# Performance work log

Hardware: AMD Instinct MI355X
Metric: run time of the kernel (lower is better)

Reference implementation:

```python
import jax, jax.numpy as jnp
import numpy as np

STRIDE = (2, 2)
PADDING = (1, 1)
OUTPUT_PADDING = (0, 0)


def setup_inputs() -> dict:
    key = jax.random.key(0)
    k1, k2, k3 = jax.random.split(key, 3)
    B, Cin, H, W = 16, 32, 128, 128
    Cout, Kh, Kw = 32, 4, 4
    signal = jax.random.normal(k1, (B, Cin, H, W), dtype=jnp.float32)
    # conv_transpose weight layout: (Cin, Cout/groups, Kh, Kw)
    weight = jax.random.normal(k2, (Cin, Cout, Kh, Kw), dtype=jnp.float32) * 0.05
    bias = jax.random.normal(k3, (Cout,), dtype=jnp.float32)
    return {"signal": signal, "weight": weight, "bias": bias}


def reference(signal, weight, bias):
    """FFT-based 2D transposed convolution (stride 2, padding 1, groups=1, dilation=1).

    Matches torch.nn.functional.conv_transpose2d semantics:
      y[n] = sum_m x[m] * w[n - m*s], cropped by `padding` on each side.
    """
    sh, sw = STRIDE
    ph, pw = PADDING
    oph, opw = OUTPUT_PADDING
    B, Cin, H, W = signal.shape
    _, Cout, Kh, Kw = weight.shape

    # 1) zero-stuff the input by the stride (lhs dilation)
    Hu, Wu = (H - 1) * sh + 1, (W - 1) * sw + 1
    xu = jnp.zeros((B, Cin, Hu, Wu), dtype=signal.dtype)
    xu = xu.at[:, :, ::sh, ::sw].set(signal)

    # 2) full (true) convolution of upsampled signal with the weight via rFFT
    Nh, Nw = Hu + Kh - 1, Wu + Kw - 1  # full-conv output size == FFT size
    Xf = jnp.fft.rfft2(xu, s=(Nh, Nw))          # (B, Cin, Nh, Nw//2+1) complex64
    Wf = jnp.fft.rfft2(weight, s=(Nh, Nw))      # (Cin, Cout, Nh, Nw//2+1) complex64
    Yf = jnp.einsum('bihw,iohw->bohw', Xf, Wf)  # contract over input channels
    y = jnp.fft.irfft2(Yf, s=(Nh, Nw))          # (B, Cout, Nh, Nw) float32

    # 3) crop by padding; output_padding extends the end (zero here)
    out_h = (H - 1) * sh - 2 * ph + Kh + oph
    out_w = (W - 1) * sw - 2 * pw + Kw + opw
    y = y[:, :, ph:ph + out_h, pw:pw + out_w]

    # 4) bias
    return y + bias[None, :, None, None]
```

## Files before the change

### kernel.cpp

```cpp
#include <hip/hip_runtime.h>

#define B_    16
#define CIN   32
#define H_    128
#define W_    128
#define COUT  32
#define OH_   256
#define OW_   256

typedef __attribute__((ext_vector_type(8))) short bf8_t;
typedef __attribute__((ext_vector_type(4))) float f32x4;

__device__ inline unsigned int f2bf(float f) {
    unsigned int u = __float_as_uint(f);
    return (u + 0x7fffu + ((u >> 16) & 1u)) >> 16;
}

__global__ __launch_bounds__(256)
void prep_w(const float* __restrict__ wgt, unsigned short* __restrict__ wt) {
    int e = blockIdx.x * 256 + threadIdx.x;
    int khkw = e >> 10, co = (e >> 5) & 31, ci = e & 31;
    wt[e] = (unsigned short)f2bf(wgt[(ci * COUT + co) * 16 + khkw]);
}

__global__ __launch_bounds__(512)
void convt_fused(const float* __restrict__ x,
                 const unsigned short* __restrict__ wt,
                 const float* __restrict__ bias,
                 float* __restrict__ y) {
    __shared__ unsigned short xs[6 * 66 * 32];

    const int tid  = threadIdx.x;
    const int lane = tid & 63;
    const int wv   = tid >> 6;
    const int n    = blockIdx.z;
    const int t0   = blockIdx.y * 4;
    const int u0   = blockIdx.x * 64;

#pragma unroll
    for (int j = 0; j < 3; ++j) {
        const int c  = wv + j * 8;
        const int hr = c >> 2, gp = c & 3;
        const int ih = t0 - 1 + hr;
        const int iw = u0 - 1 + lane;
        const bool inb = ((unsigned)ih < H_) && ((unsigned)iw < W_);
        const float* xq = x + (((long)(n * CIN + gp * 8) * H_ + ih) * W_ + iw);
        float v[8];
#pragma unroll
        for (int k = 0; k < 8; ++k)
            v[k] = inb ? xq[(long)k * (H_ * W_)] : 0.0f;
        uint4 pk;
        pk.x = f2bf(v[0]) | (f2bf(v[1]) << 16);
        pk.y = f2bf(v[2]) | (f2bf(v[3]) << 16);
        pk.z = f2bf(v[4]) | (f2bf(v[5]) << 16);
        pk.w = f2bf(v[6]) | (f2bf(v[7]) << 16);
        const int slot = gp ^ ((iw >> 1) & 3);
        *(uint4*)(xs + (hr * 66 + lane) * 32 + slot * 8) = pk;
    }
    if (tid < 48) {
        const int c  = tid >> 1;
        const int hr = c >> 2, gp = c & 3;
        const int wc = 64 + (tid & 1);
        const int ih = t0 - 1 + hr;
        const int iw = u0 - 1 + wc;
        const bool inb = ((unsigned)ih < H_) && ((unsigned)iw < W_);
        const float* xq = x + (((long)(n * CIN + gp * 8) * H_ + ih) * W_ + iw);
        float v[8];
#pragma unroll
        for (int k = 0; k < 8; ++k)
            v[k] = inb ? xq[(long)k * (H_ * W_)] : 0.0f;
        uint4 pk;
        pk.x = f2bf(v[0]) | (f2bf(v[1]) << 16);
        pk.y = f2bf(v[2]) | (f2bf(v[3]) << 16);
        pk.z = f2bf(v[4]) | (f2bf(v[5]) << 16);
        pk.w = f2bf(v[6]) | (f2bf(v[7]) << 16);
        const int slot = gp ^ ((iw >> 1) & 3);
        *(uint4*)(xs + (hr * 66 + wc) * 32 + slot * 8) = pk;
    }

    const int ch   = wv & 1;
    const int trow = wv >> 1;
    const int g    = lane >> 4;
    const int li   = lane & 15;

    bf8_t wf[16];
    {
        const unsigned short* wp = wt + (ch * 16 + li) * 32 + g * 8;
#pragma unroll
        for (int kk = 0; kk < 16; ++kk)
            wf[kk] = *(const bf8_t*)(wp + kk * 1024);
    }
    float bias4[4];
#pragma unroll
    for (int r = 0; r < 4; ++r) bias4[r] = bias[ch * 16 + g * 4 + r];

    __syncthreads();

    const int t = t0 + trow;
#pragma unroll
    for (int st = 0; st < 4; ++st) {
        const int us = u0 + st * 16;

        bf8_t xf[3][3];
#pragma unroll
        for (int dh = 0; dh < 3; ++dh) {
#pragma unroll
            for (int dw = 0; dw < 3; ++dw) {
                int wg   = us + li + dw - 1;
                int wl   = wg - (u0 - 1);
                int slot = g ^ ((wg >> 1) & 3);
                int hl   = trow + dh;
                xf[dh][dw] = *(const bf8_t*)(xs + (hl * 66 + wl) * 32 + slot * 8);
            }
        }

        f32x4 acc[2][2];
#pragma unroll
        for (int po = 0; po < 2; ++po)
#pragma unroll
            for (int qo = 0; qo < 2; ++qo)
                acc[po][qo] = (f32x4){bias4[0], bias4[1], bias4[2], bias4[3]};

#pragma unroll
        for (int po = 0; po < 2; ++po) {
            const int dh0 = po ? 2 : 1, kh0 = po ? 0 : 1;
            const int dh1 = po ? 1 : 0, kh1 = po ? 2 : 3;
#pragma unroll
            for (int qo = 0; qo < 2; ++qo) {
                const int dw0 = qo ? 2 : 1, kw0 = qo ? 0 : 1;
                const int dw1 = qo ? 1 : 0, kw1 = qo ? 2 : 3;
                acc[po][qo] = __builtin_amdgcn_mfma_f32_16x16x32_bf16(
                    wf[kh0 * 4 + kw0], xf[dh0][dw0], acc[po][qo], 0, 0, 0);
                acc[po][qo] = __builtin_amdgcn_mfma_f32_16x16x32_bf16(
                    wf[kh0 * 4 + kw1], xf[dh0][dw1], acc[po][qo], 0, 0, 0);
                acc[po][qo] = __builtin_amdgcn_mfma_f32_16x16x32_bf16(
                    wf[kh1 * 4 + kw0], xf[dh1][dw0], acc[po][qo], 0, 0, 0);
                acc[po][qo] = __builtin_amdgcn_mfma_f32_16x16x32_bf16(
                    wf[kh1 * 4 + kw1], xf[dh1][dw1], acc[po][qo], 0, 0, 0);
            }
        }

#pragma unroll
        for (int po = 0; po < 2; ++po) {
            const int oh = 2 * t + po;
#pragma unroll
            for (int r = 0; r < 4; ++r) {
                const int co = ch * 16 + g * 4 + r;
                float* yp = y + (((long)(n * COUT + co) * OH_ + oh) * OW_) + 2 * (us + li);
                *(float2*)yp = make_float2(acc[po][0][r], acc[po][1][r]);
            }
        }
    }
}

extern "C" void kernel_launch(void* const* d_in, const int* in_sizes, int n_in,
                              void* d_out, int out_size, void* d_ws, size_t ws_size,
                              hipStream_t stream) {
    const float* x = (const float*)d_in[0];
    const float* w = (const float*)d_in[1];
    const float* b = (const float*)d_in[2];
    float* y = (float*)d_out;

    unsigned short* wt = (unsigned short*)d_ws;

    prep_w<<<64, 256, 0, stream>>>(w, wt);
    convt_fused<<<dim3(W_ / 64, H_ / 4, B_), 512, 0, stream>>>(x, wt, b, y);
}
```

Before: 172.7 us.

## Swap loop order to hold half the weight fragments and cap registers

The output-row-parity loop now sits outside the spatial strip loop, so each wave keeps only 8 weight fragments (one kh pair) in registers instead of all 16. Accumulators shrink to 2 tiles, and launch bounds request 4 blocks per CU to force lower register use and higher occupancy. The cost is reloading the weight fragments from global memory twice per thread and reading the LDS input tiles twice. Output rows are also written in a different order.

```diff
diff --git a/kernel.cpp b/kernel.cpp
--- a/kernel.cpp
+++ b/kernel.cpp
@@ -23,7 +23,7 @@
     wt[e] = (unsigned short)f2bf(wgt[(ci * COUT + co) * 16 + khkw]);
 }
 
-__global__ __launch_bounds__(512)
+__global__ __launch_bounds__(512, 4)
 void convt_fused(const float* __restrict__ x,
                  const unsigned short* __restrict__ wt,
                  const float* __restrict__ bias,
@@ -83,13 +83,6 @@
     const int g    = lane >> 4;
     const int li   = lane & 15;
 
-    bf8_t wf[16];
-    {
-        const unsigned short* wp = wt + (ch * 16 + li) * 32 + g * 8;
-#pragma unroll
-        for (int kk = 0; kk < 16; ++kk)
-            wf[kk] = *(const bf8_t*)(wp + kk * 1024);
-    }
     float bias4[4];
 #pragma unroll
     for (int r = 0; r < 4; ++r) bias4[r] = bias[ch * 16 + g * 4 + r];
@@ -97,57 +90,59 @@
     __syncthreads();
 
     const int t = t0 + trow;
+    const unsigned short* wp = wt + (ch * 16 + li) * 32 + g * 8;
+
 #pragma unroll
-    for (int st = 0; st < 4; ++st) {
-        const int us = u0 + st * 16;
+    for (int po = 0; po < 2; ++po) {
+        const int kh0 = po ? 0 : 1, dh0 = po ? 2 : 1;
+        const int kh1 = po ? 2 : 3, dh1 = po ? 1 : 0;
 
-        bf8_t xf[3][3];
+        bf8_t wfA[4], wfB[4];
 #pragma unroll
-        for (int dh = 0; dh < 3; ++dh) {
+        for (int kw = 0; kw < 4; ++kw) {
+            wfA[kw] = *(const bf8_t*)(wp + (kh0 * 4 + kw) * 1024);
+            wfB[kw] = *(const bf8_t*)(wp + (kh1 * 4 + kw) * 1024);
+        }
+
+#pragma unroll
+        for (int st = 0; st < 4; ++st) {
+            const int us = u0 + st * 16;
+
+            bf8_t xfA[3], xfB[3];
 #pragma unroll
             for (int dw = 0; dw < 3; ++dw) {
-                int wg   = us + li + dw - 1;
-                int wl   = wg - (u0 - 1);
-                int slot = g ^ ((wg >> 1) & 3);
-                int hl   = trow + dh;
-                xf[dh][dw] = *(const bf8_t*)(xs + (hl * 66 + wl) * 32 + slot * 8);
+                const int wg   = us + li + dw - 1;
+                const int wl   = wg - (u0 - 1);
+                const int slot = g ^ ((wg >> 1) & 3);
+                xfA[dw] = *(const bf8_t*)(xs + ((trow + dh0) * 66 + wl) * 32 + slot * 8);
+                xfB[dw] = *(const bf8_t*)(xs + ((trow + dh1) * 66 + wl) * 32 + slot * 8);
             }
-        }
 
-        f32x4 acc[2][2];
-#pragma unroll
-        for (int po = 0; po < 2; ++po)
+            f32x4 acc[2];
 #pragma unroll
             for (int qo = 0; qo < 2; ++qo)
-                acc[po][qo] = (f32x4){bias4[0], bias4[1], bias4[2], bias4[3]};
+                acc[qo] = (f32x4){bias4[0], bias4[1], bias4[2], bias4[3]};
 
-#pragma unroll
-        for (int po = 0; po < 2; ++po) {
-            const int dh0 = po ? 2 : 1, kh0 = po ? 0 : 1;
-            const int dh1 = po ? 1 : 0, kh1 = po ? 2 : 3;
 #pragma unroll
             for (int qo = 0; qo < 2; ++qo) {
                 const int dw0 = qo ? 2 : 1, kw0 = qo ? 0 : 1;
                 const int dw1 = qo ? 1 : 0, kw1 = qo ? 2 : 3;
-                acc[po][qo] = __builtin_amdgcn_mfma_f32_16x16x32_bf16(
-                    wf[kh0 * 4 + kw0], xf[dh0][dw0], acc[po][qo], 0, 0, 0);
-                acc[po][qo] = __builtin_amdgcn_mfma_f32_16x16x32_bf16(
-                    wf[kh0 * 4 + kw1], xf[dh0][dw1], acc[po][qo], 0, 0, 0);
-                acc[po][qo] = __builtin_amdgcn_mfma_f32_16x16x32_bf16(
-                    wf[kh1 * 4 + kw0], xf[dh1][dw0], acc[po][qo], 0, 0, 0);
-                acc[po][qo] = __builtin_amdgcn_mfma_f32_16x16x32_bf16(
-                    wf[kh1 * 4 + kw1], xf[dh1][dw1], acc[po][qo], 0, 0, 0);
+                acc[qo] = __builtin_amdgcn_mfma_f32_16x16x32_bf16(
+                    wfA[kw0], xfA[dw0], acc[qo], 0, 0, 0);
+                acc[qo] = __builtin_amdgcn_mfma_f32_16x16x32_bf16(
+                    wfA[kw1], xfA[dw1], acc[qo], 0, 0, 0);
+                acc[qo] = __builtin_amdgcn_mfma_f32_16x16x32_bf16(
+                    wfB[kw0], xfB[dw0], acc[qo], 0, 0, 0);
+                acc[qo] = __builtin_amdgcn_mfma_f32_16x16x32_bf16(
+                    wfB[kw1], xfB[dw1], acc[qo], 0, 0, 0);
             }
-        }
 
-#pragma unroll
-        for (int po = 0; po < 2; ++po) {
             const int oh = 2 * t + po;
 #pragma unroll
             for (int r = 0; r < 4; ++r) {
                 const int co = ch * 16 + g * 4 + r;
                 float* yp = y + (((long)(n * COUT + co) * OH_ + oh) * OW_) + 2 * (us + li);
-                *(float2*)yp = make_float2(acc[po][0][r], acc[po][1][r]);
+                *(float2*)yp = make_float2(acc[0][r], acc[1][r]);
             }
         }
     }
```

Measured after the change: 169.2 us. 2.0% less time.
